# Kernel optimization log

Measured on AMD Instinct MI355X. Metric: run time of the kernel, lower is better.

Reference implementation:

```python
import jax, jax.numpy as jnp
import numpy as np

N_NODES = 100000
N_EDGES = 1600000
IN_F = 256
OUT_F = 64


def setup_inputs() -> dict:
    key = jax.random.key(0)
    k1, k2, k3, k4, k5 = jax.random.split(key, 5)
    features = jax.random.normal(k1, (N_NODES, IN_F), dtype=jnp.float32)
    # xavier_uniform for [in, out] weight
    limit = float(np.sqrt(6.0 / (IN_F + OUT_F)))
    weight = jax.random.uniform(k2, (IN_F, OUT_F), dtype=jnp.float32, minval=-limit, maxval=limit)
    adj_rows = jnp.sort(jax.random.randint(k3, (N_EDGES,), 0, N_NODES, dtype=jnp.int32))
    adj_cols = jax.random.randint(k4, (N_EDGES,), 0, N_NODES, dtype=jnp.int32)
    # positive edge weights (e.g. normalized adjacency values)
    adj_vals = jax.random.uniform(k5, (N_EDGES,), dtype=jnp.float32) * (1.0 / 16.0)
    return {
        "features": features,
        "weight": weight,
        "adj_rows": adj_rows,
        "adj_cols": adj_cols,
        "adj_vals": adj_vals,
        "active": 1,
    }


def _spmm(rows, cols, vals, x, n_nodes):
    # sparse [N,N] @ dense [N,F]: gather neighbor rows, scale, scatter-add
    gathered = vals[:, None] * x[cols]          # [E, F]
    return jax.ops.segment_sum(gathered, rows, num_segments=n_nodes)


def reference(features, weight, adj_rows, adj_cols, adj_vals, active):
    support = features @ weight                 # [N, out]
    if active:
        support = jnp.tanh(support)
    n = features.shape[0]
    output = _spmm(adj_rows, adj_cols, adj_vals, support, n)  # adj @ support
    az = _spmm(adj_rows, adj_cols, adj_vals, output, n)       # adj @ output
    return (output, az)
```

## Files before the change

kernel.cpp:

```cpp
#include <hip/hip_runtime.h>
#include <hip/hip_bf16.h>
#include <math.h>

#define IN_F  256
#define OUT_F 64
#define PD    264

typedef __attribute__((ext_vector_type(8))) short bf16x8;
typedef __attribute__((ext_vector_type(4))) float f32x4;

__device__ inline unsigned short f2b(float x) {
    union { __hip_bfloat16 h; unsigned short u; } cv;
    cv.h = __float2bfloat16(x);
    return cv.u;
}
__device__ inline float b2f_lo(unsigned int u) { return __uint_as_float(u << 16); }
__device__ inline float b2f_hi(unsigned int u) { return __uint_as_float(u & 0xffff0000u); }

__global__ void rowptr_kernel(const int* __restrict__ rows,
                              int* __restrict__ row_ptr,
                              int n_rows, int n_edges) {
    int r = blockIdx.x * blockDim.x + threadIdx.x;
    if (r > n_rows) return;
    if (r == n_rows) { row_ptr[n_rows] = n_edges; return; }
    int lo = 0, hi = n_edges;
    while (lo < hi) {
        int mid = (lo + hi) >> 1;
        if (rows[mid] < r) lo = mid + 1; else hi = mid;
    }
    row_ptr[r] = lo;
}

__global__ __launch_bounds__(256) void gemm_tanh_kernel(
    const float* __restrict__ feat,
    const float* __restrict__ w,
    const int*  __restrict__ active,
    unsigned short* __restrict__ sup_bf,
    int N)
{
    __shared__ unsigned short wt[OUT_F * PD];

    const int t = threadIdx.x;
    #pragma unroll
    for (int r = 0; r < 16; ++r) {
        int f = r * 256 + t;
        float4 v = ((const float4*)w)[f];
        int k = f >> 4;
        int n = (f & 15) << 2;
        wt[(n + 0) * PD + k] = f2b(v.x);
        wt[(n + 1) * PD + k] = f2b(v.y);
        wt[(n + 2) * PD + k] = f2b(v.z);
        wt[(n + 3) * PD + k] = f2b(v.w);
    }
    __syncthreads();

    const int lane = t & 63;
    const int m    = lane & 15;
    const int quad = lane >> 4;
    const int node0 = blockIdx.x * 256 + (t >> 6) * 64;

    f32x4 acc[4][4];
    #pragma unroll
    for (int a = 0; a < 4; ++a)
        #pragma unroll
        for (int b = 0; b < 4; ++b) acc[a][b] = (f32x4)0.0f;

    const float* arow[4];
    #pragma unroll
    for (int mt = 0; mt < 4; ++mt) {
        int nd = node0 + mt * 16 + m;
        if (nd > N - 1) nd = N - 1;
        arow[mt] = feat + (size_t)nd * IN_F;
    }

    for (int kt = 0; kt < 8; ++kt) {
        const int ko = kt * 32 + quad * 8;
        bf16x8 a[4];
        #pragma unroll
        for (int mt = 0; mt < 4; ++mt) {
            f32x4 lo = *(const f32x4*)(arow[mt] + ko);
            f32x4 hi = *(const f32x4*)(arow[mt] + ko + 4);
            bf16x8 av;
            av[0] = (short)f2b(lo[0]); av[1] = (short)f2b(lo[1]);
            av[2] = (short)f2b(lo[2]); av[3] = (short)f2b(lo[3]);
            av[4] = (short)f2b(hi[0]); av[5] = (short)f2b(hi[1]);
            av[6] = (short)f2b(hi[2]); av[7] = (short)f2b(hi[3]);
            a[mt] = av;
        }
        #pragma unroll
        for (int nt = 0; nt < 4; ++nt) {
            bf16x8 b = *(const bf16x8*)(&wt[(nt * 16 + m) * PD + ko]);
            #pragma unroll
            for (int mt = 0; mt < 4; ++mt)
                acc[mt][nt] = __builtin_amdgcn_mfma_f32_16x16x32_bf16(a[mt], b, acc[mt][nt], 0, 0, 0);
        }
    }

    int act = __builtin_amdgcn_readfirstlane(active[0]);
    #pragma unroll
    for (int mt = 0; mt < 4; ++mt) {
        #pragma unroll
        for (int r = 0; r < 4; ++r) {
            int node = node0 + mt * 16 + quad * 4 + r;
            if (node >= N) continue;
            #pragma unroll
            for (int nt = 0; nt < 4; ++nt) {
                float v = acc[mt][nt][r];
                if (act) v = tanhf(v);
                sup_bf[(size_t)node * OUT_F + nt * 16 + m] = f2b(v);
            }
        }
    }
}

__device__ inline int lower_bound(const int* __restrict__ a, int n, int key) {
    int lo = 0, hi = n;
    while (lo < hi) {
        int mid = (lo + hi) >> 1;
        if (a[mid] < key) lo = mid + 1; else hi = mid;
    }
    return lo;
}

template <bool XBF>
__global__ __launch_bounds__(256) void spmm_kernel(
    const int* __restrict__ row_ptr,
    const int* __restrict__ rows,
    const int* __restrict__ cols,
    const float* __restrict__ vals,
    const void* __restrict__ x,
    float* __restrict__ out,
    unsigned short* __restrict__ out_bf,
    int N, int E)
{
    const int wv   = __builtin_amdgcn_readfirstlane((int)(threadIdx.x >> 6));
    const int row  = blockIdx.x * 4 + wv;
    const int lane = threadIdx.x & 63;
    const int h    = lane >> 5;
    const int l    = lane & 31;
    if (row >= N) return;

    int s, e;
    if (row_ptr) { s = row_ptr[row]; e = row_ptr[row + 1]; }
    else         { s = lower_bound(rows, E, row); e = lower_bound(rows, E, row + 1); }

    const unsigned short* xb = (const unsigned short*)x;
    const float*          xf = (const float*)x;

    float ax = 0.0f, ay = 0.0f;
    int i = s;
    for (; i + 8 <= e; i += 8) {
        #pragma unroll
        for (int p = 0; p < 4; ++p) {
            int   c0 = cols[i + 2 * p],     c1 = cols[i + 2 * p + 1];
            float v0 = vals[i + 2 * p],     v1 = vals[i + 2 * p + 1];
            int   c  = h ? c1 : c0;
            float v  = h ? v1 : v0;
            if (XBF) {
                unsigned int r2 = *(const unsigned int*)(xb + (size_t)c * OUT_F + 2 * l);
                ax = fmaf(v, b2f_lo(r2), ax);
                ay = fmaf(v, b2f_hi(r2), ay);
            } else {
                float2 r2 = *(const float2*)(xf + (size_t)c * OUT_F + 2 * l);
                ax = fmaf(v, r2.x, ax);
                ay = fmaf(v, r2.y, ay);
            }
        }
    }
    for (; i + 2 <= e; i += 2) {
        int   c0 = cols[i],  c1 = cols[i + 1];
        float v0 = vals[i],  v1 = vals[i + 1];
        int   c  = h ? c1 : c0;
        float v  = h ? v1 : v0;
        if (XBF) {
            unsigned int r2 = *(const unsigned int*)(xb + (size_t)c * OUT_F + 2 * l);
            ax = fmaf(v, b2f_lo(r2), ax);
            ay = fmaf(v, b2f_hi(r2), ay);
        } else {
            float2 r2 = *(const float2*)(xf + (size_t)c * OUT_F + 2 * l);
            ax = fmaf(v, r2.x, ax);
            ay = fmaf(v, r2.y, ay);
        }
    }
    if (i < e) {
        int   c = cols[i];
        float v = h ? 0.0f : vals[i];
        if (XBF) {
            unsigned int r2 = *(const unsigned int*)(xb + (size_t)c * OUT_F + 2 * l);
            ax = fmaf(v, b2f_lo(r2), ax);
            ay = fmaf(v, b2f_hi(r2), ay);
        } else {
            float2 r2 = *(const float2*)(xf + (size_t)c * OUT_F + 2 * l);
            ax = fmaf(v, r2.x, ax);
            ay = fmaf(v, r2.y, ay);
        }
    }

    ax += __shfl_xor(ax, 32, 64);
    ay += __shfl_xor(ay, 32, 64);

    if (h == 0) {
        size_t base = (size_t)row * OUT_F + 2 * l;
        *(float2*)(out + base) = make_float2(ax, ay);
        if (out_bf) {
            unsigned int pk = (unsigned int)f2b(ax) | ((unsigned int)f2b(ay) << 16);
            *(unsigned int*)(out_bf + base) = pk;
        }
    }
}

extern "C" void kernel_launch(void* const* d_in, const int* in_sizes, int n_in,
                              void* d_out, int out_size, void* d_ws, size_t ws_size,
                              hipStream_t stream) {
    const float* feat   = (const float*)d_in[0];
    const float* w      = (const float*)d_in[1];
    const int*   rows   = (const int*)d_in[2];
    const int*   cols   = (const int*)d_in[3];
    const float* vals   = (const float*)d_in[4];
    const int*   active = (const int*)d_in[5];

    const int N = in_sizes[0] / IN_F;
    const int E = in_sizes[2];

    float* out = (float*)d_out;
    float* az  = out + (size_t)N * OUT_F;

    size_t rp_bytes = (((size_t)(N + 1) * sizeof(int)) + 255) & ~(size_t)255;
    size_t bf_bytes = (((size_t)N * OUT_F * sizeof(unsigned short)) + 255) & ~(size_t)255;
    char* ws = (char*)d_ws;

    int* row_ptr = (ws_size >= rp_bytes) ? (int*)ws : nullptr;
    size_t used = row_ptr ? rp_bytes : 0;

    unsigned short* sup_bf;
    unsigned short* mid_bf = nullptr;
    if (ws_size >= used + 2 * bf_bytes) {
        sup_bf = (unsigned short*)(ws + used);
        mid_bf = (unsigned short*)(ws + used + bf_bytes);
    } else if (ws_size >= used + bf_bytes) {
        sup_bf = (unsigned short*)(ws + used);
    } else {
        sup_bf = (unsigned short*)az;
    }

    if (row_ptr) {
        int threads = N + 1;
        rowptr_kernel<<<(threads + 255) / 256, 256, 0, stream>>>(rows, row_ptr, N, E);
    }

    {
        int blocks = (N + 255) / 256;
        gemm_tanh_kernel<<<blocks, 256, 0, stream>>>(feat, w, active, sup_bf, N);
    }

    int spmm_blocks = (N + 3) / 4;
    spmm_kernel<true><<<spmm_blocks, 256, 0, stream>>>(
        row_ptr, rows, cols, vals, sup_bf, out, mid_bf, N, E);
    if (mid_bf) {
        spmm_kernel<true><<<spmm_blocks, 256, 0, stream>>>(
            row_ptr, rows, cols, vals, mid_bf, az, nullptr, N, E);
    } else {
        spmm_kernel<false><<<spmm_blocks, 256, 0, stream>>>(
            row_ptr, rows, cols, vals, out, az, nullptr, N, E);
    }
}
```

Baseline: 298.5 us.

## Pre-convert weight once and shrink GEMM tile; deepen SpMM unroll

Adds a small kernel that converts and transposes the weight to bf16 in workspace once, so the GEMM blocks no longer each rebuild it in LDS. Each GEMM wave now handles 16 nodes instead of 64, with B fragments read straight from global/L2, giving more, lighter blocks and higher occupancy. The SpMM main loop is unrolled to 16 edges per iteration to keep more gathers in flight. The trade-off is repeated global reads of the weight fragments per wave and one extra kernel launch.

```diff
diff --git a/kernel.cpp b/kernel.cpp
--- a/kernel.cpp
+++ b/kernel.cpp
@@ -4,7 +4,6 @@
 
 #define IN_F  256
 #define OUT_F 64
-#define PD    264
 
 typedef __attribute__((ext_vector_type(8))) short bf16x8;
 typedef __attribute__((ext_vector_type(4))) float f32x4;
@@ -31,84 +30,61 @@
     row_ptr[r] = lo;
 }
 
-__global__ __launch_bounds__(256) void gemm_tanh_kernel(
+__global__ void wcvt_kernel(const float* __restrict__ w,
+                            unsigned short* __restrict__ wt) {
+    int t = blockIdx.x * 256 + threadIdx.x;
+    int k = t >> 6, n = t & 63;
+    wt[n * IN_F + k] = f2b(w[t]);
+}
+
+__global__ __launch_bounds__(256, 4) void gemm_tanh_kernel(
     const float* __restrict__ feat,
-    const float* __restrict__ w,
-    const int*  __restrict__ active,
+    const unsigned short* __restrict__ wt,
+    const int* __restrict__ active,
     unsigned short* __restrict__ sup_bf,
     int N)
 {
-    __shared__ unsigned short wt[OUT_F * PD];
-
-    const int t = threadIdx.x;
-    #pragma unroll
-    for (int r = 0; r < 16; ++r) {
-        int f = r * 256 + t;
-        float4 v = ((const float4*)w)[f];
-        int k = f >> 4;
-        int n = (f & 15) << 2;
-        wt[(n + 0) * PD + k] = f2b(v.x);
-        wt[(n + 1) * PD + k] = f2b(v.y);
-        wt[(n + 2) * PD + k] = f2b(v.z);
-        wt[(n + 3) * PD + k] = f2b(v.w);
-    }
-    __syncthreads();
-
-    const int lane = t & 63;
+    const int lane = threadIdx.x & 63;
     const int m    = lane & 15;
     const int quad = lane >> 4;
-    const int node0 = blockIdx.x * 256 + (t >> 6) * 64;
-
-    f32x4 acc[4][4];
+    const int node0 = (blockIdx.x * 4 + (threadIdx.x >> 6)) * 16;
+    if (node0 >= N) return;
+
+    int nd = node0 + m;
+    if (nd > N - 1) nd = N - 1;
+    const float* arow = feat + (size_t)nd * IN_F;
+
+    f32x4 acc[4];
     #pragma unroll
-    for (int a = 0; a < 4; ++a)
-        #pragma unroll
-        for (int b = 0; b < 4; ++b) acc[a][b] = (f32x4)0.0f;
-
-    const float* arow[4];
+    for (int nt = 0; nt < 4; ++nt) acc[nt] = (f32x4)0.0f;
+
     #pragma unroll
-    for (int mt = 0; mt < 4; ++mt) {
-        int nd = node0 + mt * 16 + m;
-        if (nd > N - 1) nd = N - 1;
-        arow[mt] = feat + (size_t)nd * IN_F;
-    }
-
     for (int kt = 0; kt < 8; ++kt) {
         const int ko = kt * 32 + quad * 8;
-        bf16x8 a[4];
-        #pragma unroll
-        for (int mt = 0; mt < 4; ++mt) {
-            f32x4 lo = *(const f32x4*)(arow[mt] + ko);
-            f32x4 hi = *(const f32x4*)(arow[mt] + ko + 4);
-            bf16x8 av;
-            av[0] = (short)f2b(lo[0]); av[1] = (short)f2b(lo[1]);
-            av[2] = (short)f2b(lo[2]); av[3] = (short)f2b(lo[3]);
-            av[4] = (short)f2b(hi[0]); av[5] = (short)f2b(hi[1]);
-            av[6] = (short)f2b(hi[2]); av[7] = (short)f2b(hi[3]);
-            a[mt] = av;
-        }
+        f32x4 lo = *(const f32x4*)(arow + ko);
+        f32x4 hi = *(const f32x4*)(arow + ko + 4);
+        bf16x8 a;
+        a[0] = (short)f2b(lo[0]); a[1] = (short)f2b(lo[1]);
+        a[2] = (short)f2b(lo[2]); a[3] = (short)f2b(lo[3]);
+        a[4] = (short)f2b(hi[0]); a[5] = (short)f2b(hi[1]);
+        a[6] = (short)f2b(hi[2]); a[7] = (short)f2b(hi[3]);
         #pragma unroll
         for (int nt = 0; nt < 4; ++nt) {
-            bf16x8 b = *(const bf16x8*)(&wt[(nt * 16 + m) * PD + ko]);
-            #pragma unroll
-            for (int mt = 0; mt < 4; ++mt)
-                acc[mt][nt] = __builtin_amdgcn_mfma_f32_16x16x32_bf16(a[mt], b, acc[mt][nt], 0, 0, 0);
+            bf16x8 b = *(const bf16x8*)(wt + (size_t)(nt * 16 + m) * IN_F + ko);
+            acc[nt] = __builtin_amdgcn_mfma_f32_16x16x32_bf16(a, b, acc[nt], 0, 0, 0);
         }
     }
 
     int act = __builtin_amdgcn_readfirstlane(active[0]);
     #pragma unroll
-    for (int mt = 0; mt < 4; ++mt) {
+    for (int r = 0; r < 4; ++r) {
+        int node = node0 + quad * 4 + r;
+        if (node >= N) continue;
         #pragma unroll
-        for (int r = 0; r < 4; ++r) {
-            int node = node0 + mt * 16 + quad * 4 + r;
-            if (node >= N) continue;
-            #pragma unroll
-            for (int nt = 0; nt < 4; ++nt) {
-                float v = acc[mt][nt][r];
-                if (act) v = tanhf(v);
-                sup_bf[(size_t)node * OUT_F + nt * 16 + m] = f2b(v);
-            }
+        for (int nt = 0; nt < 4; ++nt) {
+            float v = acc[nt][r];
+            if (act) v = tanhf(v);
+            sup_bf[(size_t)node * OUT_F + nt * 16 + m] = f2b(v);
         }
     }
 }
@@ -149,9 +125,9 @@
 
     float ax = 0.0f, ay = 0.0f;
     int i = s;
-    for (; i + 8 <= e; i += 8) {
+    for (; i + 16 <= e; i += 16) {
         #pragma unroll
-        for (int p = 0; p < 4; ++p) {
+        for (int p = 0; p < 8; ++p) {
             int   c0 = cols[i + 2 * p],     c1 = cols[i + 2 * p + 1];
             float v0 = vals[i + 2 * p],     v1 = vals[i + 2 * p + 1];
             int   c  = h ? c1 : c0;
@@ -226,31 +202,32 @@
     float* az  = out + (size_t)N * OUT_F;
 
     size_t rp_bytes = (((size_t)(N + 1) * sizeof(int)) + 255) & ~(size_t)255;
+    size_t wt_bytes = (((size_t)IN_F * OUT_F * sizeof(unsigned short)) + 255) & ~(size_t)255;
     size_t bf_bytes = (((size_t)N * OUT_F * sizeof(unsigned short)) + 255) & ~(size_t)255;
     char* ws = (char*)d_ws;
 
-    int* row_ptr = (ws_size >= rp_bytes) ? (int*)ws : nullptr;
-    size_t used = row_ptr ? rp_bytes : 0;
-
-    unsigned short* sup_bf;
-    unsigned short* mid_bf = nullptr;
-    if (ws_size >= used + 2 * bf_bytes) {
-        sup_bf = (unsigned short*)(ws + used);
-        mid_bf = (unsigned short*)(ws + used + bf_bytes);
-    } else if (ws_size >= used + bf_bytes) {
-        sup_bf = (unsigned short*)(ws + used);
+    int* row_ptr = nullptr;
+    unsigned short *wt, *sup_bf, *mid_bf = nullptr;
+    size_t used = 0;
+    if (ws_size >= rp_bytes) { row_ptr = (int*)ws; used += rp_bytes; }
+    if (ws_size >= used + wt_bytes + bf_bytes) {
+        wt = (unsigned short*)(ws + used); used += wt_bytes;
+        sup_bf = (unsigned short*)(ws + used); used += bf_bytes;
+        if (ws_size >= used + bf_bytes) mid_bf = (unsigned short*)(ws + used);
     } else {
-        sup_bf = (unsigned short*)az;
+        wt = (unsigned short*)az;
+        sup_bf = (unsigned short*)((char*)az + wt_bytes);
     }
 
     if (row_ptr) {
         int threads = N + 1;
         rowptr_kernel<<<(threads + 255) / 256, 256, 0, stream>>>(rows, row_ptr, N, E);
     }
+    wcvt_kernel<<<(IN_F * OUT_F) / 256, 256, 0, stream>>>(w, wt);
 
     {
-        int blocks = (N + 255) / 256;
-        gemm_tanh_kernel<<<blocks, 256, 0, stream>>>(feat, w, active, sup_bf, N);
+        int blocks = (N + 63) / 64;
+        gemm_tanh_kernel<<<blocks, 256, 0, stream>>>(feat, wt, active, sup_bf, N);
     }
 
     int spmm_blocks = (N + 3) / 4;
```

Result: slower. 309.0 us (+3.5%).
